# Kernel optimization log

Hardware: AMD Instinct MI355X
Metric: run time of the kernel (lower is better)

## Reference

```python
import jax, jax.numpy as jnp
import numpy as np

B, N, E = 16, 1024, 32768
HEADS, OC = 4, 8          # GATConv: out_channels = d_out // heads = 8
D_IN, A_DIM = 33, 8
DM, DO = 16, 32
EPS_LN = 1e-5


def setup_inputs() -> dict:
    key = jax.random.key(0)
    ks = jax.random.split(key, 24)
    r = lambda k, s: (0.1 * jax.random.normal(k, s)).astype(jnp.float32)
    return {
        "H": jax.random.normal(ks[0], (B, N, D_IN + A_DIM + 1), dtype=jnp.float32),
        "edge_index": jax.random.randint(ks[1], (2, E), 0, N, dtype=jnp.int32),
        "fc_s_w": r(ks[2], (DM, D_IN)), "fc_s_b": r(ks[3], (DM,)),
        "fc_a_w": r(ks[4], (DM, A_DIM)), "fc_a_b": r(ks[5], (DM,)),
        "fc_r_w": r(ks[6], (DM, 1)), "fc_r_b": r(ks[7], (DM,)),
        "fuse_q": r(ks[8], (3, DM)),
        "fuse_k_w": r(ks[9], (DM, DM)),
        "fuse_v_w": r(ks[10], (DM, DM)),
        "proj_w": r(ks[11], (DO, DM)), "proj_b": r(ks[12], (DO,)),
        "post_w": r(ks[13], (DO, DO)), "post_b": r(ks[14], (DO,)),
        "ln_g": jnp.ones((DO,), jnp.float32), "ln_b": jnp.zeros((DO,), jnp.float32),
        "gat_w": r(ks[15], (HEADS * OC, DO)),
        "att_src": r(ks[16], (HEADS, OC)),
        "att_dst": r(ks[17], (HEADS, OC)),
        "gat_b": r(ks[18], (HEADS * OC,)),
    }


def reference(H, edge_index, fc_s_w, fc_s_b, fc_a_w, fc_a_b, fc_r_w, fc_r_b,
              fuse_q, fuse_k_w, fuse_v_w, proj_w, proj_b, post_w, post_b,
              ln_g, ln_b, gat_w, att_src, att_dst, gat_b):
    # ---- ObsEmbedding: split obs | prev-action | prev-reward, embed to DM ----
    s = H[..., :D_IN]
    a = H[..., D_IN:D_IN + A_DIM]
    rr = H[..., D_IN + A_DIM:]
    tok = jnp.stack([s @ fc_s_w.T + fc_s_b,
                     a @ fc_a_w.T + fc_a_b,
                     rr @ fc_r_w.T + fc_r_b], axis=-2)            # [B,N,3,DM]
    K = tok @ fuse_k_w.T
    V = tok @ fuse_v_w.T
    attn = jnp.einsum('qd,bntd->bnqt', fuse_q, K) / jnp.sqrt(jnp.float32(DM))
    w = jax.nn.softmax(attn, axis=-1)                             # [B,N,3,3]
    fused = jnp.einsum('bnqt,bntd->bnqd', w, V).mean(-2)          # [B,N,DM]
    z = jax.nn.relu(fused) @ proj_w.T + proj_b                    # [B,N,DO]
    h = jax.nn.relu(z @ post_w.T + post_b)
    mu = h.mean(-1, keepdims=True)
    var = ((h - mu) ** 2).mean(-1, keepdims=True)
    Hn = (h - mu) / jnp.sqrt(var + EPS_LN) * ln_g + ln_b          # [B,N,DO]

    # ---- GATConv (eval mode: dropout off, add_self_loops=False) ----
    src, dst = edge_index[0], edge_index[1]
    x = (Hn @ gat_w.T).reshape(B, N, HEADS, OC)                   # [B,N,H,OC]
    a_s = (x * att_src).sum(-1)                                   # [B,N,H]
    a_d = (x * att_dst).sum(-1)
    e = jax.nn.leaky_relu(a_s[:, src] + a_d[:, dst], 0.2)         # [B,E,H]

    def per_graph(e_b, x_b):
        # scatter-softmax over incoming edges of each destination node
        m = jax.ops.segment_max(e_b, dst, num_segments=N)
        ex = jnp.exp(e_b - m[dst])
        den = jax.ops.segment_sum(ex, dst, num_segments=N)
        alpha = ex / den[dst]                                     # [E,H]
        out = jax.ops.segment_sum(alpha[:, :, None] * x_b[src], dst,
                                  num_segments=N)                 # [N,H,OC]
        A = jnp.zeros((HEADS, N, N), jnp.float32).at[:, src, dst].add(alpha.T)
        A = A / jnp.maximum(A.sum(-1, keepdims=True), 1e-9)
        return out.reshape(N, HEADS * OC) + gat_b, A

    out, A = jax.vmap(per_graph)(e, x)                            # [B,N,32], [B,H,N,N]
    return out, A
```

## Files before the change

kernel.cpp:

```cpp
#include <hip/hip_runtime.h>
#include <math.h>

namespace {

constexpr int B = 16, N = 1024, E = 32768, HEADS = 4, OC = 8;
constexpr int D_IN = 33, A_DIM = 8, DM = 16, DO = 32;
constexpr int F = D_IN + A_DIM + 1;
constexpr int BCAP = 256;
constexpr int FILLB = E / 256;

typedef float f4 __attribute__((ext_vector_type(4)));

__device__ __forceinline__ float lrelu(float x) { return x >= 0.f ? x : 0.2f * x; }

__global__ __launch_bounds__(256) void k_prep(
    const int* __restrict__ ei, int* __restrict__ cnt_src,
    int* __restrict__ cnt_dst, int* __restrict__ bkt_src,
    int* __restrict__ bkt_dst,
    const float* __restrict__ H,
    const float* __restrict__ fc_s_w, const float* __restrict__ fc_s_b,
    const float* __restrict__ fc_a_w, const float* __restrict__ fc_a_b,
    const float* __restrict__ fc_r_w, const float* __restrict__ fc_r_b,
    const float* __restrict__ fuse_q, const float* __restrict__ fuse_k_w,
    const float* __restrict__ fuse_v_w, const float* __restrict__ proj_w,
    const float* __restrict__ proj_b, const float* __restrict__ post_w,
    const float* __restrict__ post_b, const float* __restrict__ ln_g,
    const float* __restrict__ ln_b, const float* __restrict__ gat_w,
    const float* __restrict__ att_src, const float* __restrict__ att_dst,
    float* __restrict__ x_out, float* __restrict__ as_out, float* __restrict__ advi) {
  if (blockIdx.x < FILLB) {
    int e = blockIdx.x * 256 + threadIdx.x;
    int s = ei[e], d = ei[E + e];
    int p1 = atomicAdd(&cnt_src[s], 1);
    if (p1 < BCAP) bkt_src[s * BCAP + p1] = d;
    int p2 = atomicAdd(&cnt_dst[d], 1);
    if (p2 < BCAP) bkt_dst[d * BCAP + p2] = s;
    return;
  }
  int node = (blockIdx.x - FILLB) * 256 + threadIdx.x;
  if (node >= B * N) return;

  const float* hin = H + (size_t)node * F;
  float hv[F];
#pragma unroll
  for (int i = 0; i < F; i++) hv[i] = hin[i];

  float tok[3][DM];
#pragma unroll
  for (int j = 0; j < DM; j++) {
    float acc = fc_s_b[j];
#pragma unroll
    for (int i = 0; i < D_IN; i++) acc = fmaf(hv[i], fc_s_w[j * D_IN + i], acc);
    tok[0][j] = acc;
    float acc2 = fc_a_b[j];
#pragma unroll
    for (int i = 0; i < A_DIM; i++) acc2 = fmaf(hv[D_IN + i], fc_a_w[j * A_DIM + i], acc2);
    tok[1][j] = acc2;
    tok[2][j] = fmaf(hv[F - 1], fc_r_w[j], fc_r_b[j]);
  }

  float Kf[3][DM], Vf[3][DM];
#pragma unroll
  for (int t = 0; t < 3; t++) {
#pragma unroll
    for (int j = 0; j < DM; j++) {
      float ak = 0.f, av = 0.f;
#pragma unroll
      for (int d = 0; d < DM; d++) {
        ak = fmaf(tok[t][d], fuse_k_w[j * DM + d], ak);
        av = fmaf(tok[t][d], fuse_v_w[j * DM + d], av);
      }
      Kf[t][j] = ak; Vf[t][j] = av;
    }
  }

  float wbar[3] = {0.f, 0.f, 0.f};
#pragma unroll
  for (int q = 0; q < 3; q++) {
    float att[3];
#pragma unroll
    for (int t = 0; t < 3; t++) {
      float acc = 0.f;
#pragma unroll
      for (int d = 0; d < DM; d++) acc = fmaf(fuse_q[q * DM + d], Kf[t][d], acc);
      att[t] = acc * 0.25f;
    }
    float mx = fmaxf(att[0], fmaxf(att[1], att[2]));
    float e0 = expf(att[0] - mx), e1 = expf(att[1] - mx), e2 = expf(att[2] - mx);
    float inv = 1.f / (e0 + e1 + e2);
    wbar[0] += e0 * inv; wbar[1] += e1 * inv; wbar[2] += e2 * inv;
  }

  float fused[DM];
#pragma unroll
  for (int d = 0; d < DM; d++) {
    float f = (wbar[0] * Vf[0][d] + wbar[1] * Vf[1][d] + wbar[2] * Vf[2][d]) * (1.f / 3.f);
    fused[d] = fmaxf(f, 0.f);
  }

  float z[DO];
#pragma unroll
  for (int o = 0; o < DO; o++) {
    float acc = proj_b[o];
#pragma unroll
    for (int d = 0; d < DM; d++) acc = fmaf(fused[d], proj_w[o * DM + d], acc);
    z[o] = acc;
  }

  float h2[DO]; float mu = 0.f;
#pragma unroll
  for (int o = 0; o < DO; o++) {
    float acc = post_b[o];
#pragma unroll
    for (int d = 0; d < DO; d++) acc = fmaf(z[d], post_w[o * DO + d], acc);
    acc = fmaxf(acc, 0.f);
    h2[o] = acc; mu += acc;
  }
  mu *= (1.f / DO);
  float var = 0.f;
#pragma unroll
  for (int o = 0; o < DO; o++) { float dd = h2[o] - mu; var = fmaf(dd, dd, var); }
  var *= (1.f / DO);
  float rstd = rsqrtf(var + 1e-5f);
  float Hn[DO];
#pragma unroll
  for (int o = 0; o < DO; o++) Hn[o] = fmaf((h2[o] - mu) * rstd, ln_g[o], ln_b[o]);

  float* xrow = x_out + (size_t)node * (HEADS * OC);
  f4 asv, adv;
#pragma unroll
  for (int hh = 0; hh < HEADS; hh++) {
    float as = 0.f, ad = 0.f;
#pragma unroll
    for (int oc = 0; oc < OC; oc++) {
      int k = hh * OC + oc;
      float acc = 0.f;
#pragma unroll
      for (int d = 0; d < DO; d++) acc = fmaf(Hn[d], gat_w[k * DO + d], acc);
      xrow[k] = acc;
      as = fmaf(acc, att_src[k], as);
      ad = fmaf(acc, att_dst[k], ad);
    }
    asv[hh] = as; adv[hh] = ad;
  }
  *(f4*)(as_out + (size_t)node * HEADS) = asv;
  *(f4*)(advi + (size_t)node * 8) = adv;
}

__global__ __launch_bounds__(256) void k_inv(
    const int* __restrict__ cnt_dst, const int* __restrict__ bkt_dst,
    const float* __restrict__ as_, float* __restrict__ advi) {
  int w = threadIdx.x >> 6, lane = threadIdx.x & 63;
  int bd = blockIdx.x * 4 + w;
  int b = bd >> 10, dn = bd & (N - 1);
  int deg = min(cnt_dst[dn], BCAP);
  const int* list = bkt_dst + dn * BCAP;

  f4 adv = *(const f4*)(advi + (size_t)(b * N + dn) * 8);

  float sm0 = 0.f, sm1 = 0.f, sm2 = 0.f, sm3 = 0.f;
  for (int i = lane; i < deg; i += 64) {
    int s = list[i];
    f4 ap = *(const f4*)(as_ + (size_t)(b * N + s) * HEADS);
    sm0 += __expf(lrelu(ap.x + adv.x));
    sm1 += __expf(lrelu(ap.y + adv.y));
    sm2 += __expf(lrelu(ap.z + adv.z));
    sm3 += __expf(lrelu(ap.w + adv.w));
  }
#pragma unroll
  for (int off = 1; off < 64; off <<= 1) {
    sm0 += __shfl_xor(sm0, off);
    sm1 += __shfl_xor(sm1, off);
    sm2 += __shfl_xor(sm2, off);
    sm3 += __shfl_xor(sm3, off);
  }
  f4 inv;
  inv.x = sm0 > 0.f ? 1.f / sm0 : 0.f;
  inv.y = sm1 > 0.f ? 1.f / sm1 : 0.f;
  inv.z = sm2 > 0.f ? 1.f / sm2 : 0.f;
  inv.w = sm3 > 0.f ? 1.f / sm3 : 0.f;
  if (lane == 0) *(f4*)(advi + (size_t)(b * N + dn) * 8 + 4) = inv;
}

__global__ __launch_bounds__(256) void k_outA(
    const int* __restrict__ cnt_src, const int* __restrict__ bkt_src,
    const int* __restrict__ cnt_dst, const int* __restrict__ bkt_dst,
    const float* __restrict__ as_, const float* __restrict__ advi,
    const float* __restrict__ x_, const float* __restrict__ gat_b,
    float* __restrict__ out, float* __restrict__ A) {
  __shared__ float row[HEADS][N];
  int bs = blockIdx.x;
  int s = bs & (N - 1);
  int b = bs >> 10;
  int h = threadIdx.x >> 6, lane = threadIdx.x & 63;

  f4* rowv = (f4*)row[h];
#pragma unroll
  for (int j = 0; j < 4; j++) rowv[lane + j * 64] = (f4){0.f, 0.f, 0.f, 0.f};
  __syncthreads();

  float as_h = as_[(size_t)(b * N + s) * HEADS + h];
  int degO = min(cnt_src[s], BCAP);
  const int* listO = bkt_src + s * BCAP;
  float r = 0.f;
  for (int i = lane; i < degO; i += 64) {
    int d = listO[i];
    const float* rec = advi + (size_t)(b * N + d) * 8;
    float a = __expf(lrelu(as_h + rec[h])) * rec[4 + h];
    atomicAdd(&row[h][d], a);
    r += a;
  }
#pragma unroll
  for (int off = 1; off < 64; off <<= 1) r += __shfl_xor(r, off);

  {
    int degI = min(cnt_dst[s], BCAP);
    const int* listI = bkt_dst + s * BCAP;
    float adh = advi[(size_t)(b * N + s) * 8 + h];
    float ivh = advi[(size_t)(b * N + s) * 8 + 4 + h];
    int eslot = lane >> 3, cl = lane & 7, c = h * OC + cl;
    float acc = 0.f;
    for (int i = eslot; i < degI; i += 8) {
      int src = listI[i];
      float ex = __expf(lrelu(as_[(size_t)(b * N + src) * HEADS + h] + adh));
      acc = fmaf(ex, x_[(size_t)(b * N + src) * (HEADS * OC) + c], acc);
    }
    acc += __shfl_xor(acc, 8);
    acc += __shfl_xor(acc, 16);
    acc += __shfl_xor(acc, 32);
    if (eslot == 0)
      out[(size_t)bs * (HEADS * OC) + c] = acc * ivh + gat_b[c];
  }

  __syncthreads();

  float ivr = 1.f / fmaxf(r, 1e-9f);
  float* Arow = A + (((size_t)b * HEADS + h) * N + s) * N;
#pragma unroll
  for (int j = 0; j < 4; j++) {
    f4 v = rowv[lane + j * 64];
    v.x *= ivr; v.y *= ivr; v.z *= ivr; v.w *= ivr;
    __builtin_nontemporal_store(v, (f4*)Arow + lane + j * 64);
  }
}

}

extern "C" void kernel_launch(void* const* d_in, const int* in_sizes, int n_in,
                              void* d_out, int out_size, void* d_ws, size_t ws_size,
                              hipStream_t stream) {
  const float* H      = (const float*)d_in[0];
  const int*   ei     = (const int*)  d_in[1];
  const float* fc_s_w = (const float*)d_in[2];
  const float* fc_s_b = (const float*)d_in[3];
  const float* fc_a_w = (const float*)d_in[4];
  const float* fc_a_b = (const float*)d_in[5];
  const float* fc_r_w = (const float*)d_in[6];
  const float* fc_r_b = (const float*)d_in[7];
  const float* fuse_q = (const float*)d_in[8];
  const float* fuse_k_w = (const float*)d_in[9];
  const float* fuse_v_w = (const float*)d_in[10];
  const float* proj_w = (const float*)d_in[11];
  const float* proj_b = (const float*)d_in[12];
  const float* post_w = (const float*)d_in[13];
  const float* post_b = (const float*)d_in[14];
  const float* ln_g   = (const float*)d_in[15];
  const float* ln_b   = (const float*)d_in[16];
  const float* gat_w  = (const float*)d_in[17];
  const float* att_src = (const float*)d_in[18];
  const float* att_dst = (const float*)d_in[19];
  const float* gat_b  = (const float*)d_in[20];

  float* out = (float*)d_out;
  float* A   = out + (size_t)B * N * DO;

  float* ws   = (float*)d_ws;
  float* xbuf = ws;
  float* asb  = xbuf + (size_t)B * N * (HEADS * OC);
  float* advi = asb + (size_t)B * N * HEADS;
  int* ibase   = (int*)(advi + (size_t)B * N * 8);
  int* cnt_src = ibase;
  int* cnt_dst = cnt_src + N;
  int* bkt_src = cnt_dst + N;
  int* bkt_dst = bkt_src + N * BCAP;

  (void)hipMemsetAsync(cnt_src, 0, 2 * N * sizeof(int), stream);
  k_prep<<<dim3(FILLB + (B * N) / 256), dim3(256), 0, stream>>>(
      ei, cnt_src, cnt_dst, bkt_src, bkt_dst,
      H, fc_s_w, fc_s_b, fc_a_w, fc_a_b, fc_r_w, fc_r_b, fuse_q, fuse_k_w,
      fuse_v_w, proj_w, proj_b, post_w, post_b, ln_g, ln_b, gat_w, att_src,
      att_dst, xbuf, asb, advi);

  k_inv<<<dim3(B * N / 4), dim3(256), 0, stream>>>(cnt_dst, bkt_dst, asb, advi);

  k_outA<<<dim3(B * N), dim3(256), 0, stream>>>(cnt_src, bkt_src, cnt_dst, bkt_dst,
                                                asb, advi, xbuf, gat_b, out, A);
}
```

Before: 118.5 us.

## Process eight batch rows per block sharing node adjacency lists; interleave ad/inv layout

The A/out kernel now handles 8 consecutive (batch,node) rows per block, ordered so the rows share the same node and differ only in batch. Degree counts and bucket lists are loaded once and reused across those rows, and per-block launch overhead drops. The advi record is interleaved as (ad, inv) pairs per head so a single 8-byte load fetches both. The cost is fewer blocks, which lowers parallelism and serialises the A-row writes inside each block, and the outer loop adds extra __syncthreads.

```diff
diff --git a/kernel.cpp b/kernel.cpp
--- a/kernel.cpp
+++ b/kernel.cpp
@@ -8,10 +8,13 @@
 constexpr int F = D_IN + A_DIM + 1;
 constexpr int BCAP = 256;
 constexpr int FILLB = E / 256;
+constexpr int ROWS_PER_BLK = 8;
 
 typedef float f4 __attribute__((ext_vector_type(4)));
+typedef float f2 __attribute__((ext_vector_type(2)));
 
 __device__ __forceinline__ float lrelu(float x) { return x >= 0.f ? x : 0.2f * x; }
+
 
 __global__ __launch_bounds__(256) void k_prep(
     const int* __restrict__ ei, int* __restrict__ cnt_src,
@@ -127,7 +130,7 @@
   for (int o = 0; o < DO; o++) Hn[o] = fmaf((h2[o] - mu) * rstd, ln_g[o], ln_b[o]);
 
   float* xrow = x_out + (size_t)node * (HEADS * OC);
-  f4 asv, adv;
+  f4 asv;
 #pragma unroll
   for (int hh = 0; hh < HEADS; hh++) {
     float as = 0.f, ad = 0.f;
@@ -141,31 +144,32 @@
       as = fmaf(acc, att_src[k], as);
       ad = fmaf(acc, att_dst[k], ad);
     }
-    asv[hh] = as; adv[hh] = ad;
+    asv[hh] = as;
+    advi[(size_t)node * 8 + 2 * hh] = ad;
   }
   *(f4*)(as_out + (size_t)node * HEADS) = asv;
-  *(f4*)(advi + (size_t)node * 8) = adv;
 }
 
 __global__ __launch_bounds__(256) void k_inv(
     const int* __restrict__ cnt_dst, const int* __restrict__ bkt_dst,
     const float* __restrict__ as_, float* __restrict__ advi) {
   int w = threadIdx.x >> 6, lane = threadIdx.x & 63;
-  int bd = blockIdx.x * 4 + w;
-  int b = bd >> 10, dn = bd & (N - 1);
+  int r = blockIdx.x * 4 + w;
+  int b = r & (B - 1), dn = r >> 4;
   int deg = min(cnt_dst[dn], BCAP);
   const int* list = bkt_dst + dn * BCAP;
 
-  f4 adv = *(const f4*)(advi + (size_t)(b * N + dn) * 8);
+  const float* adp = advi + (size_t)(b * N + dn) * 8;
+  float a0 = adp[0], a1 = adp[2], a2 = adp[4], a3 = adp[6];
 
   float sm0 = 0.f, sm1 = 0.f, sm2 = 0.f, sm3 = 0.f;
   for (int i = lane; i < deg; i += 64) {
     int s = list[i];
     f4 ap = *(const f4*)(as_ + (size_t)(b * N + s) * HEADS);
-    sm0 += __expf(lrelu(ap.x + adv.x));
-    sm1 += __expf(lrelu(ap.y + adv.y));
-    sm2 += __expf(lrelu(ap.z + adv.z));
-    sm3 += __expf(lrelu(ap.w + adv.w));
+    sm0 += __expf(lrelu(ap.x + a0));
+    sm1 += __expf(lrelu(ap.y + a1));
+    sm2 += __expf(lrelu(ap.z + a2));
+    sm3 += __expf(lrelu(ap.w + a3));
   }
 #pragma unroll
   for (int off = 1; off < 64; off <<= 1) {
@@ -174,12 +178,13 @@
     sm2 += __shfl_xor(sm2, off);
     sm3 += __shfl_xor(sm3, off);
   }
-  f4 inv;
-  inv.x = sm0 > 0.f ? 1.f / sm0 : 0.f;
-  inv.y = sm1 > 0.f ? 1.f / sm1 : 0.f;
-  inv.z = sm2 > 0.f ? 1.f / sm2 : 0.f;
-  inv.w = sm3 > 0.f ? 1.f / sm3 : 0.f;
-  if (lane == 0) *(f4*)(advi + (size_t)(b * N + dn) * 8 + 4) = inv;
+  if (lane == 0) {
+    float* ivp = advi + (size_t)(b * N + dn) * 8 + 1;
+    ivp[0] = sm0 > 0.f ? 1.f / sm0 : 0.f;
+    ivp[2] = sm1 > 0.f ? 1.f / sm1 : 0.f;
+    ivp[4] = sm2 > 0.f ? 1.f / sm2 : 0.f;
+    ivp[6] = sm3 > 0.f ? 1.f / sm3 : 0.f;
+  }
 }
 
 __global__ __launch_bounds__(256) void k_outA(
@@ -189,58 +194,62 @@
     const float* __restrict__ x_, const float* __restrict__ gat_b,
     float* __restrict__ out, float* __restrict__ A) {
   __shared__ float row[HEADS][N];
-  int bs = blockIdx.x;
-  int s = bs & (N - 1);
-  int b = bs >> 10;
   int h = threadIdx.x >> 6, lane = threadIdx.x & 63;
-
   f4* rowv = (f4*)row[h];
-#pragma unroll
-  for (int j = 0; j < 4; j++) rowv[lane + j * 64] = (f4){0.f, 0.f, 0.f, 0.f};
-  __syncthreads();
-
-  float as_h = as_[(size_t)(b * N + s) * HEADS + h];
+
+  int r0 = blockIdx.x * ROWS_PER_BLK;
+  int s = r0 >> 4;
   int degO = min(cnt_src[s], BCAP);
   const int* listO = bkt_src + s * BCAP;
-  float r = 0.f;
-  for (int i = lane; i < degO; i += 64) {
-    int d = listO[i];
-    const float* rec = advi + (size_t)(b * N + d) * 8;
-    float a = __expf(lrelu(as_h + rec[h])) * rec[4 + h];
-    atomicAdd(&row[h][d], a);
-    r += a;
-  }
-#pragma unroll
-  for (int off = 1; off < 64; off <<= 1) r += __shfl_xor(r, off);
-
-  {
-    int degI = min(cnt_dst[s], BCAP);
-    const int* listI = bkt_dst + s * BCAP;
-    float adh = advi[(size_t)(b * N + s) * 8 + h];
-    float ivh = advi[(size_t)(b * N + s) * 8 + 4 + h];
-    int eslot = lane >> 3, cl = lane & 7, c = h * OC + cl;
-    float acc = 0.f;
-    for (int i = eslot; i < degI; i += 8) {
-      int src = listI[i];
-      float ex = __expf(lrelu(as_[(size_t)(b * N + src) * HEADS + h] + adh));
-      acc = fmaf(ex, x_[(size_t)(b * N + src) * (HEADS * OC) + c], acc);
-    }
-    acc += __shfl_xor(acc, 8);
-    acc += __shfl_xor(acc, 16);
-    acc += __shfl_xor(acc, 32);
-    if (eslot == 0)
-      out[(size_t)bs * (HEADS * OC) + c] = acc * ivh + gat_b[c];
-  }
-
-  __syncthreads();
-
-  float ivr = 1.f / fmaxf(r, 1e-9f);
-  float* Arow = A + (((size_t)b * HEADS + h) * N + s) * N;
-#pragma unroll
-  for (int j = 0; j < 4; j++) {
-    f4 v = rowv[lane + j * 64];
-    v.x *= ivr; v.y *= ivr; v.z *= ivr; v.w *= ivr;
-    __builtin_nontemporal_store(v, (f4*)Arow + lane + j * 64);
+  int degI = min(cnt_dst[s], BCAP);
+  const int* listI = bkt_dst + s * BCAP;
+  float gb = gat_b[h * OC + (lane & 7)];
+
+  for (int r = r0; r < r0 + ROWS_PER_BLK; ++r) {
+    int b = r & (B - 1);
+
+#pragma unroll
+    for (int j = 0; j < 4; j++) rowv[lane + j * 64] = (f4){0.f, 0.f, 0.f, 0.f};
+    __syncthreads();
+
+    float as_h = as_[(size_t)(b * N + s) * HEADS + h];
+    float rs = 0.f;
+    for (int i = lane; i < degO; i += 64) {
+      int d = listO[i];
+      f2 rec = *(const f2*)(advi + (size_t)(b * N + d) * 8 + 2 * h);
+      float a = __expf(lrelu(as_h + rec.x)) * rec.y;
+      atomicAdd(&row[h][d], a);
+      rs += a;
+    }
+#pragma unroll
+    for (int off = 1; off < 64; off <<= 1) rs += __shfl_xor(rs, off);
+
+    {
+      f2 self = *(const f2*)(advi + (size_t)(b * N + s) * 8 + 2 * h);
+      int eslot = lane >> 3, cl = lane & 7, c = h * OC + cl;
+      float acc = 0.f;
+      for (int i = eslot; i < degI; i += 8) {
+        int src = listI[i];
+        float ex = __expf(lrelu(as_[(size_t)(b * N + src) * HEADS + h] + self.x));
+        acc = fmaf(ex, x_[(size_t)(b * N + src) * (HEADS * OC) + c], acc);
+      }
+      acc += __shfl_xor(acc, 8);
+      acc += __shfl_xor(acc, 16);
+      acc += __shfl_xor(acc, 32);
+      if (eslot == 0)
+        out[(size_t)(b * N + s) * (HEADS * OC) + c] = acc * self.y + gb;
+    }
+
+    __syncthreads();
+
+    float ivr = 1.f / fmaxf(rs, 1e-9f);
+    float* Arow = A + (((size_t)b * HEADS + h) * N + s) * N;
+#pragma unroll
+    for (int j = 0; j < 4; j++) {
+      f4 v = rowv[lane + j * 64];
+      v.x *= ivr; v.y *= ivr; v.z *= ivr; v.w *= ivr;
+      __builtin_nontemporal_store(v, (f4*)Arow + lane + j * 64);
+    }
   }
 }
 
@@ -293,6 +302,6 @@
 
   k_inv<<<dim3(B * N / 4), dim3(256), 0, stream>>>(cnt_dst, bkt_dst, asb, advi);
 
-  k_outA<<<dim3(B * N), dim3(256), 0, stream>>>(cnt_src, bkt_src, cnt_dst, bkt_dst,
-                                                asb, advi, xbuf, gat_b, out, A);
-}
+  k_outA<<<dim3(B * N / ROWS_PER_BLK), dim3(256), 0, stream>>>(
+      cnt_src, bkt_src, cnt_dst, bkt_dst, asb, advi, xbuf, gat_b, out, A);
+}
```

New measurement: 106.5 us. -10.1%, faster.
